# Optimization experiments

Hardware: AMD Instinct MI355X
Metric: run time of the kernel (lower is better)

Reference implementation:

```python
import jax, jax.numpy as jnp
import numpy as np

S, N, C, E, L = 4, 50000, 256, 800000, 3
EPS = 1e-5  # nn.LayerNorm default eps


def setup_inputs() -> dict:
    key = jax.random.key(0)
    ks = jax.random.split(key, 10)
    sc = 1.0 / np.sqrt(C)
    x = jax.random.normal(ks[0], (S, N, C), jnp.float32)
    edge_index = jax.random.randint(ks[1], (S, 2, E), 0, N, dtype=jnp.int32)
    edge_weight = jax.random.uniform(ks[2], (S, E), jnp.float32)
    W_gcn = jax.random.uniform(ks[3], (L, C, C), jnp.float32, -sc, sc)
    b_gcn = jnp.zeros((L, C), jnp.float32)
    ln_scale = jnp.ones((L, C), jnp.float32)
    ln_bias = jnp.zeros((L, C), jnp.float32)
    w_ih = jax.random.uniform(ks[4], (3 * C, C), jnp.float32, -sc, sc)
    w_hh = jax.random.uniform(ks[5], (3 * C, C), jnp.float32, -sc, sc)
    b_ih = jax.random.uniform(ks[6], (3 * C,), jnp.float32, -sc, sc)
    b_hh = jax.random.uniform(ks[7], (3 * C,), jnp.float32, -sc, sc)
    return dict(x=x, edge_index=edge_index, edge_weight=edge_weight,
                W_gcn=W_gcn, b_gcn=b_gcn, ln_scale=ln_scale, ln_bias=ln_bias,
                w_ih=w_ih, w_hh=w_hh, b_ih=b_ih, b_hh=b_hh)


def _gcn_conv(h, row, col, ew, W, b):
    """PyG GCNConv: out = D^{-1/2} (A + I) D^{-1/2} (h W) + b, edge weights ew."""
    h = h @ W  # [N, C]
    loop = jnp.arange(N, dtype=row.dtype)
    row = jnp.concatenate([row, loop])
    col = jnp.concatenate([col, loop])
    ew = jnp.concatenate([ew, jnp.ones((N,), ew.dtype)])
    deg = jax.ops.segment_sum(ew, col, num_segments=N)  # in-degree at targets
    dinv = jnp.where(deg > 0, jax.lax.rsqrt(jnp.maximum(deg, EPS * 0 + 1e-12)), 0.0)
    norm = dinv[row] * ew * dinv[col]  # [E+N]
    msg = h[row] * norm[:, None]       # gather from sources
    return jax.ops.segment_sum(msg, col, num_segments=N) + b


def _layernorm(h, scale, bias):
    mu = jnp.mean(h, axis=-1, keepdims=True)
    var = jnp.mean(jnp.square(h - mu), axis=-1, keepdims=True)
    return (h - mu) * jax.lax.rsqrt(var + EPS) * scale + bias


def _snapshot(x, ei, ew, W_gcn, b_gcn, ln_scale, ln_bias):
    h = x
    row, col = ei[0], ei[1]
    for l in range(L):
        h = _gcn_conv(h, row, col, ew, W_gcn[l], b_gcn[l])
        h = _layernorm(h, ln_scale[l], ln_bias[l])
        h = jax.nn.relu(h)  # dropout is identity in eval mode
    return h


def _gru_last(seq, w_ih, w_hh, b_ih, b_hh):
    """seq: [S, N, C] -> final hidden [N, C] (torch single-layer GRU)."""
    def step(h, x_t):
        gi = x_t @ w_ih.T + b_ih
        gh = h @ w_hh.T + b_hh
        i_r, i_z, i_n = jnp.split(gi, 3, axis=-1)
        h_r, h_z, h_n = jnp.split(gh, 3, axis=-1)
        r = jax.nn.sigmoid(i_r + h_r)
        z = jax.nn.sigmoid(i_z + h_z)
        n = jnp.tanh(i_n + r * h_n)
        return (1.0 - z) * n + z * h, None
    h0 = jnp.zeros(seq.shape[1:], seq.dtype)
    h_last, _ = jax.lax.scan(step, h0, seq)
    return h_last


def reference(x, edge_index, edge_weight, W_gcn, b_gcn, ln_scale, ln_bias,
              w_ih, w_hh, b_ih, b_hh):
    feats = jax.vmap(lambda xs, eis, ews: _snapshot(xs, eis, ews, W_gcn, b_gcn, ln_scale, ln_bias))(
        x, edge_index, edge_weight)  # [S, N, C]
    return _gru_last(feats, w_ih, w_hh, b_ih, b_hh)  # [N, C]
```

## Files before the change

kernel.cpp:

```cpp
#include <hip/hip_runtime.h>
#include <cmath>

#define S_ 4
#define N_ 50000
#define C_ 256
#define E_ 800000
#define L_ 3
#define EPS_ 1e-5f
#define NCH_ ((N_ + 1023) / 1024)

typedef __attribute__((ext_vector_type(8))) short bf16x8;
typedef __attribute__((ext_vector_type(4))) float f32x4;

__device__ __forceinline__ float bf2f(unsigned short s) {
  return __uint_as_float(((unsigned)s) << 16);
}
__device__ __forceinline__ unsigned short f2bf(float f) {
  unsigned u = __float_as_uint(f);
  return (unsigned short)((u + 0x7fffu + ((u >> 16) & 1u)) >> 16);
}

__device__ __forceinline__ void gload_lds16(const void* g, void* l) {
  __builtin_amdgcn_global_load_lds(
      (const __attribute__((address_space(1))) unsigned int*)g,
      (__attribute__((address_space(3))) unsigned int*)l, 16, 0, 0);
}

__device__ __forceinline__ void swz_block(int id, int nbx, int nby, int& bmi, int& bni) {
  const int NB8 = nby * 8;
  int fullb = (nbx >> 3) * NB8;
  if (id < fullb) {
    int g = id / NB8, pp = id - g * NB8;
    bmi = g * 8 + (pp & 7);
    bni = pp >> 3;
  } else {
    int rem = nbx & 7;
    int idp = id - fullb;
    bmi = (nbx & ~7) + idp % rem;
    bni = idp / rem;
  }
}

__global__ __launch_bounds__(256) void gemm_bf16_kernel(
    const unsigned short* __restrict__ A, const unsigned short* __restrict__ Bt,
    unsigned short* __restrict__ Cout, int M, int Nn, int K, int nby)
{
  __shared__ alignas(16) unsigned short As[2][128 * 32];
  __shared__ alignas(16) unsigned short Bs[2][128 * 32];
  const int tid = threadIdx.x;
  const int lane = tid & 63;
  const int wid = tid >> 6;
  const int wr = wid >> 1, wc = wid & 1;
  int bmi, bni;
  swz_block(blockIdx.x, gridDim.x / nby, nby, bmi, bni);
  const int bm = bmi * 128, bn = bni * 128;
  const int l15 = lane & 15, l4 = lane >> 4;

  f32x4 acc[4][4] = {};

  int offA[4], offB[4];
  #pragma unroll
  for (int mi = 0; mi < 4; ++mi) {
    int ra = wr * 64 + mi * 16 + l15;
    offA[mi] = ra * 32 + ((l4 ^ ((ra >> 1) & 3)) << 3);
    int rb = wc * 64 + mi * 16 + l15;
    offB[mi] = rb * 32 + ((l4 ^ ((rb >> 1) & 3)) << 3);
  }
  const int rs = tid >> 2;
  const int gs = tid & 3;

  auto stage = [&](int buf, int k0) {
    #pragma unroll
    for (int t2 = 0; t2 < 2; ++t2) {
      int r = rs + t2 * 64;
      int q = gs ^ ((r >> 1) & 3);
      int arow = bm + r; if (arow >= M) arow = M - 1;
      gload_lds16(&A[(size_t)arow * K + k0 + q * 8], &As[buf][(t2 * 256 + tid) * 8]);
      int brow = bn + r;
      gload_lds16(&Bt[(size_t)brow * K + k0 + q * 8], &Bs[buf][(t2 * 256 + tid) * 8]);
    }
  };

  const int nt = K >> 5;
  stage(0, 0);
  asm volatile("s_waitcnt vmcnt(0)" ::: "memory");
  __syncthreads();

  int cur = 0;
  for (int t = 0; t < nt; ++t) {
    if (t + 1 < nt) stage(cur ^ 1, (t + 1) * 32);

    bf16x8 af[4], bfr[4];
    #pragma unroll
    for (int mi = 0; mi < 4; ++mi) af[mi] = *(const bf16x8*)&As[cur][offA[mi]];
    #pragma unroll
    for (int ni = 0; ni < 4; ++ni) bfr[ni] = *(const bf16x8*)&Bs[cur][offB[ni]];
    #pragma unroll
    for (int mi = 0; mi < 4; ++mi)
      #pragma unroll
      for (int ni = 0; ni < 4; ++ni)
        acc[mi][ni] = __builtin_amdgcn_mfma_f32_16x16x32_bf16(
            af[mi], bfr[ni], acc[mi][ni], 0, 0, 0);

    asm volatile("s_waitcnt vmcnt(0)" ::: "memory");
    __syncthreads();
    cur ^= 1;
  }

  #pragma unroll
  for (int mi = 0; mi < 4; ++mi) {
    int rowb = bm + wr * 64 + mi * 16 + l4 * 4;
    #pragma unroll
    for (int ni = 0; ni < 4; ++ni) {
      int col = bn + wc * 64 + ni * 16 + l15;
      #pragma unroll
      for (int r = 0; r < 4; ++r) {
        int row = rowb + r;
        if (row < M) Cout[(size_t)row * Nn + col] = f2bf(acc[mi][ni][r]);
      }
    }
  }
}

__global__ __launch_bounds__(256) void gru_fused_kernel(
    const unsigned short* __restrict__ feat,
    const unsigned short* __restrict__ hq_in,
    const unsigned short* __restrict__ Wp_ih,
    const unsigned short* __restrict__ Wp_hh,
    const float* __restrict__ b_ih, const float* __restrict__ b_hh,
    unsigned short* __restrict__ hq_out, float* __restrict__ hout,
    int first, int M)
{
  __shared__ alignas(16) unsigned short As[2][128 * 32];
  __shared__ alignas(16) unsigned short Bs[2][96 * 32];
  const int tid = threadIdx.x;
  const int lane = tid & 63;
  const int wv = tid >> 6;
  const int l15 = lane & 15, l4 = lane >> 4;

  int bmi, bni;
  swz_block(blockIdx.x, gridDim.x / 8, 8, bmi, bni);
  const int bm = bmi * 128;
  const int c0 = bni * 32;
  const int brow0 = bni * 96;

  f32x4 acc_i[2][6] = {};
  f32x4 acc_h[2][6] = {};

  int offA[2], offB[6];
  #pragma unroll
  for (int mi = 0; mi < 2; ++mi) {
    int ra = wv * 32 + mi * 16 + l15;
    offA[mi] = ra * 32 + ((l4 ^ ((ra >> 1) & 3)) << 3);
  }
  #pragma unroll
  for (int ni = 0; ni < 6; ++ni) {
    int rb = ni * 16 + l15;
    offB[ni] = rb * 32 + ((l4 ^ ((rb >> 1) & 3)) << 3);
  }

  const int nt = first ? 8 : 16;

  auto stage = [&](int buf, int t) {
    int k0 = (t & 7) * 32;
    const unsigned short* Ap = (t < 8) ? feat : hq_in;
    const unsigned short* Bp = (t < 8) ? Wp_ih : Wp_hh;
    #pragma unroll
    for (int t2 = 0; t2 < 2; ++t2) {
      int slot = t2 * 256 + tid;
      int r = slot >> 2;
      int q = (slot & 3) ^ ((r >> 1) & 3);
      int arow = bm + r; if (arow >= M) arow = M - 1;
      gload_lds16(&Ap[(size_t)arow * 256 + k0 + q * 8], &As[buf][slot * 8]);
    }
    {
      int slot = tid;
      int r = slot >> 2;
      int q = (slot & 3) ^ ((r >> 1) & 3);
      gload_lds16(&Bp[(size_t)(brow0 + r) * 256 + k0 + q * 8], &Bs[buf][slot * 8]);
    }
    if (tid < 128) {
      int slot = 256 + tid;
      int r = slot >> 2;
      int q = (slot & 3) ^ ((r >> 1) & 3);
      gload_lds16(&Bp[(size_t)(brow0 + r) * 256 + k0 + q * 8], &Bs[buf][slot * 8]);
    }
  };

  stage(0, 0);
  asm volatile("s_waitcnt vmcnt(0)" ::: "memory");
  __syncthreads();

  int cur = 0;
  for (int t = 0; t < nt; ++t) {
    if (t + 1 < nt) stage(cur ^ 1, t + 1);

    bf16x8 af[2], bfr[6];
    #pragma unroll
    for (int mi = 0; mi < 2; ++mi) af[mi] = *(const bf16x8*)&As[cur][offA[mi]];
    #pragma unroll
    for (int ni = 0; ni < 6; ++ni) bfr[ni] = *(const bf16x8*)&Bs[cur][offB[ni]];
    if (t < 8) {
      #pragma unroll
      for (int mi = 0; mi < 2; ++mi)
        #pragma unroll
        for (int ni = 0; ni < 6; ++ni)
          acc_i[mi][ni] = __builtin_amdgcn_mfma_f32_16x16x32_bf16(
              af[mi], bfr[ni], acc_i[mi][ni], 0, 0, 0);
    } else {
      #pragma unroll
      for (int mi = 0; mi < 2; ++mi)
        #pragma unroll
        for (int ni = 0; ni < 6; ++ni)
          acc_h[mi][ni] = __builtin_amdgcn_mfma_f32_16x16x32_bf16(
              af[mi], bfr[ni], acc_h[mi][ni], 0, 0, 0);
    }

    asm volatile("s_waitcnt vmcnt(0)" ::: "memory");
    __syncthreads();
    cur ^= 1;
  }

  #pragma unroll
  for (int cni = 0; cni < 2; ++cni) {
    int c = c0 + cni * 16 + l15;
    float bir = b_ih[c], biz = b_ih[256 + c], bin = b_ih[512 + c];
    float bhr = b_hh[c], bhz = b_hh[256 + c], bhn = b_hh[512 + c];
    #pragma unroll
    for (int mi = 0; mi < 2; ++mi) {
      int rowb = bm + wv * 32 + mi * 16 + l4 * 4;
      #pragma unroll
      for (int rr = 0; rr < 4; ++rr) {
        int row = rowb + rr;
        if (row < M) {
          float gir = acc_i[mi][0 + cni][rr] + bir;
          float ghr = acc_h[mi][0 + cni][rr] + bhr;
          float giz = acc_i[mi][2 + cni][rr] + biz;
          float ghz = acc_h[mi][2 + cni][rr] + bhz;
          float gin = acc_i[mi][4 + cni][rr] + bin;
          float ghn = acc_h[mi][4 + cni][rr] + bhn;
          float rg = 1.f / (1.f + expf(-(gir + ghr)));
          float zg = 1.f / (1.f + expf(-(giz + ghz)));
          float ng = tanhf(gin + rg * ghn);
          float hp = first ? 0.f : bf2f(hq_in[(size_t)row * 256 + c]);
          float hv = (1.f - zg) * ng + zg * hp;
          if (hq_out) hq_out[(size_t)row * 256 + c] = f2bf(hv);
          if (hout) hout[(size_t)row * 256 + c] = hv;
        }
      }
    }
  }
}

__global__ void prep_wgcn_kernel(const float* __restrict__ W, unsigned short* __restrict__ Wt) {
  int i = blockIdx.x * blockDim.x + threadIdx.x;
  if (i < L_ * C_ * C_) {
    int l = i / (C_ * C_);
    int rem = i - l * C_ * C_;
    int nn = rem >> 8, k = rem & 255;
    Wt[i] = f2bf(W[l * C_ * C_ + k * C_ + nn]);
  }
}
__global__ void prep_wp_kernel(const float* __restrict__ W, unsigned short* __restrict__ Wp) {
  int d = blockIdx.x * blockDim.x + threadIdx.x;
  if (d < 768 * 256) {
    int jrow = d >> 8, k = d & 255;
    int chunk = jrow / 96, j = jrow - chunk * 96;
    int g = j >> 5, dc = j & 31;
    int srow = g * 256 + chunk * 32 + dc;
    Wp[d] = f2bf(W[srow * 256 + k]);
  }
}
__global__ void quant_kernel(const float* __restrict__ in, unsigned short* __restrict__ out, int n4) {
  int i = blockIdx.x * blockDim.x + threadIdx.x;
  if (i < n4) {
    float4 v = ((const float4*)in)[i];
    ushort4 q;
    q.x = f2bf(v.x); q.y = f2bf(v.y); q.z = f2bf(v.z); q.w = f2bf(v.w);
    *(ushort4*)&out[i * 4] = q;
  }
}

__global__ void init_kernel(unsigned long long* __restrict__ deg64,
                            int* __restrict__ fill, int n) {
  int i = blockIdx.x * blockDim.x + threadIdx.x;
  if (i < n) { deg64[i] = (1ULL << 20); fill[i] = 0; }
}
__global__ void deg_count_all_kernel(const int* __restrict__ edge_idx,
                                     const float* __restrict__ edge_w,
                                     unsigned long long* __restrict__ deg64) {
  int e = blockIdx.x * blockDim.x + threadIdx.x;
  if (e < S_ * E_) {
    int s = e / E_;
    int ee = e - s * E_;
    int c = edge_idx[(size_t)s * 2 * E_ + E_ + ee];
    float w = edge_w[(size_t)s * E_ + ee];
    unsigned long long q = (unsigned long long)__float2uint_rn(w * 1048576.0f);
    atomicAdd(&deg64[s * N_ + c], q + (1ULL << 40));
  }
}
__global__ void dinv_kernel(const unsigned long long* __restrict__ deg64,
                            float* __restrict__ dinv, int n) {
  int i = blockIdx.x * blockDim.x + threadIdx.x;
  if (i < n) {
    float d = (float)(deg64[i] & ((1ULL << 40) - 1)) * (1.0f / 1048576.0f);
    dinv[i] = rsqrtf(fmaxf(d, 1e-12f));
  }
}
__global__ void chunk_sum_kernel(const unsigned long long* __restrict__ deg64,
                                 int* __restrict__ chunk_sum) {
  int b = blockIdx.x;
  int s = b / NCH_, ch = b - s * NCH_;
  const unsigned long long* dg = deg64 + (size_t)s * N_;
  int base = ch * 1024 + threadIdx.x * 4;
  int v = 0;
  #pragma unroll
  for (int j = 0; j < 4; ++j)
    if (base + j < N_) v += (int)(dg[base + j] >> 40);
  #pragma unroll
  for (int off = 32; off > 0; off >>= 1) v += __shfl_down(v, off);
  __shared__ int ws[4];
  int lane = threadIdx.x & 63, wv = threadIdx.x >> 6;
  if (lane == 0) ws[wv] = v;
  __syncthreads();
  if (threadIdx.x == 0) chunk_sum[s * NCH_ + ch] = ws[0] + ws[1] + ws[2] + ws[3];
}
__global__ void scan_chunks_kernel(int* __restrict__ chunk_sum, int* __restrict__ rowptr) {
  int s = threadIdx.x;
  if (s < S_) {
    int tot = 0;
    for (int ch = 0; ch < NCH_; ++ch) {
      int t = chunk_sum[s * NCH_ + ch];
      chunk_sum[s * NCH_ + ch] = tot;
      tot += t;
    }
    rowptr[s * (N_ + 1) + N_] = tot;
  }
}
__global__ void scan_final_kernel(const unsigned long long* __restrict__ deg64,
                                  const int* __restrict__ chunk_sum,
                                  int* __restrict__ rowptr) {
  int b = blockIdx.x;
  int s = b / NCH_, ch = b - s * NCH_;
  const unsigned long long* dg = deg64 + (size_t)s * N_;
  int t = threadIdx.x;
  int i0 = ch * 1024 + t * 4;
  int c0 = 0, c1 = 0, c2 = 0, c3 = 0;
  if (i0 + 0 < N_) c0 = (int)(dg[i0 + 0] >> 40);
  if (i0 + 1 < N_) c1 = (int)(dg[i0 + 1] >> 40);
  if (i0 + 2 < N_) c2 = (int)(dg[i0 + 2] >> 40);
  if (i0 + 3 < N_) c3 = (int)(dg[i0 + 3] >> 40);
  int tsum = c0 + c1 + c2 + c3;
  int lane = t & 63, wv = t >> 6;
  int inc = tsum;
  #pragma unroll
  for (int off = 1; off < 64; off <<= 1) {
    int u = __shfl_up(inc, off);
    if (lane >= off) inc += u;
  }
  __shared__ int ws[4];
  if (lane == 63) ws[wv] = inc;
  __syncthreads();
  int woff = 0;
  for (int k = 0; k < 4; ++k) if (k < wv) woff += ws[k];
  int off0 = chunk_sum[s * NCH_ + ch] + woff + inc - tsum;
  int* rp = rowptr + (size_t)s * (N_ + 1);
  if (i0 + 0 < N_) rp[i0 + 0] = off0;
  if (i0 + 1 < N_) rp[i0 + 1] = off0 + c0;
  if (i0 + 2 < N_) rp[i0 + 2] = off0 + c0 + c1;
  if (i0 + 3 < N_) rp[i0 + 3] = off0 + c0 + c1 + c2;
}
__global__ void csr_fill_all_kernel(const int* __restrict__ edge_idx,
                                    const float* __restrict__ edge_w,
                                    const float* __restrict__ dinv,
                                    const int* __restrict__ rowptr, int* __restrict__ fill,
                                    unsigned int* __restrict__ src_norm) {
  int e = blockIdx.x * blockDim.x + threadIdx.x;
  if (e < S_ * E_) {
    int s = e / E_;
    int ee = e - s * E_;
    int r = edge_idx[(size_t)s * 2 * E_ + ee];
    int c = edge_idx[(size_t)s * 2 * E_ + E_ + ee];
    float w = edge_w[(size_t)s * E_ + ee];
    int pos = rowptr[s * (N_ + 1) + c] + atomicAdd(&fill[s * N_ + c], 1);
    float nrm = dinv[s * N_ + r] * w * dinv[s * N_ + c];
    unsigned int rec = (unsigned int)r | ((unsigned int)f2bf(nrm) << 16);
    src_norm[(size_t)s * E_ + pos] = rec;
  }
}

__global__ __launch_bounds__(256) void spmm_ln_relu_kernel(
    const unsigned short* __restrict__ hW, const int* __restrict__ rowptr,
    const unsigned int* __restrict__ src_norm,
    const float* __restrict__ dinv, const float* __restrict__ bgcn,
    const float* __restrict__ lnsc, const float* __restrict__ lnbi,
    unsigned short* __restrict__ out)
{
  const int tid = threadIdx.x;
  const int lane = tid & 63, wv = tid >> 6;
  const int n = blockIdx.x * 4 + wv;
  const int c4 = lane << 2;

  float a0, a1, a2, a3;
  {
    float dv = dinv[n];
    float w = dv * dv;
    ushort4 u = *(const ushort4*)&hW[((size_t)n << 8) + c4];
    a0 = w * bf2f(u.x); a1 = w * bf2f(u.y); a2 = w * bf2f(u.z); a3 = w * bf2f(u.w);
  }
  const int e0 = rowptr[n], e1 = rowptr[n + 1];
  for (int base = e0; base < e1; base += 64) {
    int cnt = min(64, e1 - base);
    unsigned int rec = (base + lane < e1) ? src_norm[base + lane] : 0u;
    int j = 0;
    for (; j + 3 < cnt; j += 4) {
      unsigned int r0 = __shfl((int)rec, j + 0);
      unsigned int r1 = __shfl((int)rec, j + 1);
      unsigned int r2 = __shfl((int)rec, j + 2);
      unsigned int r3 = __shfl((int)rec, j + 3);
      ushort4 u0 = *(const ushort4*)&hW[((size_t)(r0 & 0xFFFFu) << 8) + c4];
      ushort4 u1 = *(const ushort4*)&hW[((size_t)(r1 & 0xFFFFu) << 8) + c4];
      ushort4 u2 = *(const ushort4*)&hW[((size_t)(r2 & 0xFFFFu) << 8) + c4];
      ushort4 u3 = *(const ushort4*)&hW[((size_t)(r3 & 0xFFFFu) << 8) + c4];
      float n0 = bf2f((unsigned short)(r0 >> 16));
      float n1 = bf2f((unsigned short)(r1 >> 16));
      float n2 = bf2f((unsigned short)(r2 >> 16));
      float n3 = bf2f((unsigned short)(r3 >> 16));
      a0 = fmaf(n0, bf2f(u0.x), a0); a1 = fmaf(n0, bf2f(u0.y), a1);
      a2 = fmaf(n0, bf2f(u0.z), a2); a3 = fmaf(n0, bf2f(u0.w), a3);
      a0 = fmaf(n1, bf2f(u1.x), a0); a1 = fmaf(n1, bf2f(u1.y), a1);
      a2 = fmaf(n1, bf2f(u1.z), a2); a3 = fmaf(n1, bf2f(u1.w), a3);
      a0 = fmaf(n2, bf2f(u2.x), a0); a1 = fmaf(n2, bf2f(u2.y), a1);
      a2 = fmaf(n2, bf2f(u2.z), a2); a3 = fmaf(n2, bf2f(u2.w), a3);
      a0 = fmaf(n3, bf2f(u3.x), a0); a1 = fmaf(n3, bf2f(u3.y), a1);
      a2 = fmaf(n3, bf2f(u3.z), a2); a3 = fmaf(n3, bf2f(u3.w), a3);
    }
    for (; j < cnt; ++j) {
      unsigned int r0 = __shfl((int)rec, j);
      ushort4 u0 = *(const ushort4*)&hW[((size_t)(r0 & 0xFFFFu) << 8) + c4];
      float n0 = bf2f((unsigned short)(r0 >> 16));
      a0 = fmaf(n0, bf2f(u0.x), a0); a1 = fmaf(n0, bf2f(u0.y), a1);
      a2 = fmaf(n0, bf2f(u0.z), a2); a3 = fmaf(n0, bf2f(u0.w), a3);
    }
  }

  float4 bg = *(const float4*)&bgcn[c4];
  float v0 = a0 + bg.x, v1 = a1 + bg.y, v2 = a2 + bg.z, v3 = a3 + bg.w;
  float s1 = (v0 + v1) + (v2 + v3);
  float s2 = (v0 * v0 + v1 * v1) + (v2 * v2 + v3 * v3);
  #pragma unroll
  for (int off = 32; off > 0; off >>= 1) {
    s1 += __shfl_xor(s1, off);
    s2 += __shfl_xor(s2, off);
  }
  float mu = s1 * (1.0f / C_);
  float var = s2 * (1.0f / C_) - mu * mu;
  float inv = rsqrtf(var + EPS_);
  float4 sc = *(const float4*)&lnsc[c4];
  float4 bi = *(const float4*)&lnbi[c4];
  ushort4 o;
  o.x = f2bf(fmaxf((v0 - mu) * inv * sc.x + bi.x, 0.f));
  o.y = f2bf(fmaxf((v1 - mu) * inv * sc.y + bi.y, 0.f));
  o.z = f2bf(fmaxf((v2 - mu) * inv * sc.z + bi.z, 0.f));
  o.w = f2bf(fmaxf((v3 - mu) * inv * sc.w + bi.w, 0.f));
  *(ushort4*)&out[((size_t)n << 8) + c4] = o;
}

extern "C" void kernel_launch(void* const* d_in, const int* in_sizes, int n_in,
                              void* d_out, int out_size, void* d_ws, size_t ws_size,
                              hipStream_t stream) {
  const float* x        = (const float*)d_in[0];
  const int*   edge_idx = (const int*)d_in[1];
  const float* edge_w   = (const float*)d_in[2];
  const float* W_gcn    = (const float*)d_in[3];
  const float* b_gcn    = (const float*)d_in[4];
  const float* ln_scale = (const float*)d_in[5];
  const float* ln_bias  = (const float*)d_in[6];
  const float* w_ih     = (const float*)d_in[7];
  const float* w_hh     = (const float*)d_in[8];
  const float* b_ih     = (const float*)d_in[9];
  const float* b_hh     = (const float*)d_in[10];
  float* h_out = (float*)d_out;

  char* p = (char*)d_ws;
  auto carve = [&](size_t bytes) -> void* {
    void* r = (void*)p;
    p += (bytes + 255) & ~(size_t)255;
    return r;
  };
  unsigned long long* deg64 = (unsigned long long*)carve((size_t)S_ * N_ * 8);
  float* dinv        = (float*)carve((size_t)S_ * N_ * 4);
  int*   fill        = (int*)carve((size_t)S_ * N_ * 4);
  int*   rowptr      = (int*)carve((size_t)S_ * (N_ + 1) * 4);
  int*   chunk_sum   = (int*)carve((size_t)S_ * NCH_ * 4);
  unsigned int* src_norm = (unsigned int*)carve((size_t)S_ * E_ * 4);
  unsigned short* wt_gcn = (unsigned short*)carve((size_t)L_ * C_ * C_ * 2);
  unsigned short* wp_ih  = (unsigned short*)carve((size_t)768 * C_ * 2);
  unsigned short* wp_hh  = (unsigned short*)carve((size_t)768 * C_ * 2);
  unsigned short* xq_all = (unsigned short*)carve((size_t)S_ * N_ * C_ * 2);
  unsigned short* hW_all = (unsigned short*)carve((size_t)S_ * N_ * C_ * 2);
  unsigned short* fA_all = (unsigned short*)carve((size_t)S_ * N_ * C_ * 2);
  unsigned short* hq0    = (unsigned short*)carve((size_t)N_ * C_ * 2);
  unsigned short* hq1    = (unsigned short*)carve((size_t)N_ * C_ * 2);

  const int TB = 256;

  prep_wgcn_kernel<<<(L_ * C_ * C_ + TB - 1) / TB, TB, 0, stream>>>(W_gcn, wt_gcn);
  prep_wp_kernel<<<(768 * C_ + TB - 1) / TB, TB, 0, stream>>>(w_ih, wp_ih);
  prep_wp_kernel<<<(768 * C_ + TB - 1) / TB, TB, 0, stream>>>(w_hh, wp_hh);

  quant_kernel<<<((size_t)S_ * N_ * C_ / 4 + TB - 1) / TB, TB, 0, stream>>>(
      x, xq_all, S_ * N_ * C_ / 4);

  init_kernel<<<(S_ * N_ + TB - 1) / TB, TB, 0, stream>>>(deg64, fill, S_ * N_);
  deg_count_all_kernel<<<(S_ * E_ + TB - 1) / TB, TB, 0, stream>>>(edge_idx, edge_w, deg64);
  dinv_kernel<<<(S_ * N_ + TB - 1) / TB, TB, 0, stream>>>(deg64, dinv, S_ * N_);
  chunk_sum_kernel<<<S_ * NCH_, TB, 0, stream>>>(deg64, chunk_sum);
  scan_chunks_kernel<<<1, 64, 0, stream>>>(chunk_sum, rowptr);
  scan_final_kernel<<<S_ * NCH_, TB, 0, stream>>>(deg64, chunk_sum, rowptr);
  csr_fill_all_kernel<<<(S_ * E_ + TB - 1) / TB, TB, 0, stream>>>(
      edge_idx, edge_w, dinv, rowptr, fill, src_norm);

  const int M_all = S_ * N_;
  const int nbx = (M_all + 127) / 128;
  {
    const unsigned short* hin = xq_all;
    for (int l = 0; l < L_; ++l) {
      unsigned short* fout = (l == 1) ? xq_all : fA_all;
      gemm_bf16_kernel<<<nbx * (C_ / 128), 256, 0, stream>>>(
          hin, wt_gcn + (size_t)l * C_ * C_, hW_all, M_all, C_, C_, C_ / 128);
      for (int s = 0; s < S_; ++s) {
        spmm_ln_relu_kernel<<<N_ / 4, 256, 0, stream>>>(
            hW_all + (size_t)s * N_ * C_, rowptr + s * (N_ + 1),
            src_norm + (size_t)s * E_,
            dinv + s * N_, b_gcn + l * C_,
            ln_scale + l * C_, ln_bias + l * C_, fout + (size_t)s * N_ * C_);
      }
      hin = fout;
    }
  }
  const unsigned short* feat_all = fA_all;

  const int gnb = ((N_ + 127) / 128) * 8;
  unsigned short* hq_cur = hq0;
  unsigned short* hq_nxt = hq1;
  for (int s = 0; s < S_; ++s) {
    bool last = (s == S_ - 1);
    gru_fused_kernel<<<gnb, 256, 0, stream>>>(
        feat_all + (size_t)s * N_ * C_,
        hq_cur,
        wp_ih, wp_hh, b_ih, b_hh,
        last ? nullptr : hq_nxt,
        last ? h_out : nullptr,
        (s == 0) ? 1 : 0, N_);
    unsigned short* t = hq_cur; hq_cur = hq_nxt; hq_nxt = t;
  }
}
```

Baseline: 1.678 ms.

## Build CSR via column-bucketed binning with shared-memory atomics; batch SpMM across snapshots

Replaces the global-atomic degree count and CSR fill with a two-pass bucket sort. Edges are first binned by column block into per-bucket sub-bins. Per-bucket kernels then count degrees and fill CSR positions using LDS atomics, and compute dinv locally. The four per-snapshot SpMM launches are also merged into one launch over all snapshots. This costs a large fixed-capacity bin buffer and silently drops edges if a sub-bin overflows CAP8.

```diff
diff --git a/kernel.cpp b/kernel.cpp
--- a/kernel.cpp
+++ b/kernel.cpp
@@ -8,6 +8,11 @@
 #define L_ 3
 #define EPS_ 1e-5f
 #define NCH_ ((N_ + 1023) / 1024)
+#define BKT_SH 9
+#define BKT_SZ 512
+#define NBKT ((N_ + BKT_SZ - 1) / BKT_SZ)
+#define NSUB 8
+#define CAP8 2048
 
 typedef __attribute__((ext_vector_type(8))) short bf16x8;
 typedef __attribute__((ext_vector_type(4))) float f32x4;
@@ -281,42 +286,70 @@
   }
 }
 
-__global__ void init_kernel(unsigned long long* __restrict__ deg64,
-                            int* __restrict__ fill, int n) {
-  int i = blockIdx.x * blockDim.x + threadIdx.x;
-  if (i < n) { deg64[i] = (1ULL << 20); fill[i] = 0; }
-}
-__global__ void deg_count_all_kernel(const int* __restrict__ edge_idx,
-                                     const float* __restrict__ edge_w,
-                                     unsigned long long* __restrict__ deg64) {
+__global__ void bin_kernel(const int* __restrict__ edge_idx,
+                           const float* __restrict__ edge_w,
+                           unsigned long long* __restrict__ bins,
+                           int* __restrict__ bfill) {
   int e = blockIdx.x * blockDim.x + threadIdx.x;
   if (e < S_ * E_) {
     int s = e / E_;
     int ee = e - s * E_;
+    int r = edge_idx[(size_t)s * 2 * E_ + ee];
     int c = edge_idx[(size_t)s * 2 * E_ + E_ + ee];
     float w = edge_w[(size_t)s * E_ + ee];
-    unsigned long long q = (unsigned long long)__float2uint_rn(w * 1048576.0f);
-    atomicAdd(&deg64[s * N_ + c], q + (1ULL << 40));
-  }
-}
-__global__ void dinv_kernel(const unsigned long long* __restrict__ deg64,
-                            float* __restrict__ dinv, int n) {
-  int i = blockIdx.x * blockDim.x + threadIdx.x;
-  if (i < n) {
-    float d = (float)(deg64[i] & ((1ULL << 40) - 1)) * (1.0f / 1048576.0f);
-    dinv[i] = rsqrtf(fmaxf(d, 1e-12f));
-  }
-}
-__global__ void chunk_sum_kernel(const unsigned long long* __restrict__ deg64,
+    int sb = (s * NBKT + (c >> BKT_SH)) * NSUB + (blockIdx.x & (NSUB - 1));
+    int pos = atomicAdd(&bfill[sb], 1);
+    if (pos < CAP8) {
+      unsigned long long rec = ((unsigned long long)__float_as_uint(w) << 32)
+          | (unsigned int)(r | ((c & (BKT_SZ - 1)) << 16));
+      bins[(size_t)sb * CAP8 + pos] = rec;
+    }
+  }
+}
+
+__global__ __launch_bounds__(256) void bucket_stats_kernel(
+    const unsigned long long* __restrict__ bins, const int* __restrict__ bfill,
+    int* __restrict__ cnt_g, float* __restrict__ dinv_g) {
+  __shared__ unsigned int lcnt[BKT_SZ], lwd[BKT_SZ];
+  int b = blockIdx.x;
+  int s = b / NBKT, bl = b - s * NBKT;
+  int col0 = bl << BKT_SH;
+  for (int i = threadIdx.x; i < BKT_SZ; i += 256) { lcnt[i] = 0; lwd[i] = 0; }
+  __syncthreads();
+  for (int sub = 0; sub < NSUB; ++sub) {
+    int sb = b * NSUB + sub;
+    int nb = min(bfill[sb], CAP8);
+    const unsigned long long* bp = bins + (size_t)sb * CAP8;
+    for (int e = threadIdx.x; e < nb; e += 256) {
+      unsigned long long rec = bp[e];
+      unsigned int lo = (unsigned int)rec;
+      int cl = (lo >> 16) & (BKT_SZ - 1);
+      float w = __uint_as_float((unsigned int)(rec >> 32));
+      atomicAdd(&lcnt[cl], 1u);
+      atomicAdd(&lwd[cl], (unsigned int)__float2uint_rn(w * 1048576.0f));
+    }
+  }
+  __syncthreads();
+  for (int i = threadIdx.x; i < BKT_SZ; i += 256) {
+    int c = col0 + i;
+    if (c < N_) {
+      cnt_g[s * N_ + c] = (int)lcnt[i];
+      float d = (float)lwd[i] * (1.0f / 1048576.0f) + 1.0f;
+      dinv_g[s * N_ + c] = rsqrtf(d);
+    }
+  }
+}
+
+__global__ void chunk_sum_kernel(const int* __restrict__ cnt_g,
                                  int* __restrict__ chunk_sum) {
   int b = blockIdx.x;
   int s = b / NCH_, ch = b - s * NCH_;
-  const unsigned long long* dg = deg64 + (size_t)s * N_;
+  const int* cs = cnt_g + (size_t)s * N_;
   int base = ch * 1024 + threadIdx.x * 4;
   int v = 0;
   #pragma unroll
   for (int j = 0; j < 4; ++j)
-    if (base + j < N_) v += (int)(dg[base + j] >> 40);
+    if (base + j < N_) v += cs[base + j];
   #pragma unroll
   for (int off = 32; off > 0; off >>= 1) v += __shfl_down(v, off);
   __shared__ int ws[4];
@@ -337,19 +370,19 @@
     rowptr[s * (N_ + 1) + N_] = tot;
   }
 }
-__global__ void scan_final_kernel(const unsigned long long* __restrict__ deg64,
+__global__ void scan_final_kernel(const int* __restrict__ cnt_g,
                                   const int* __restrict__ chunk_sum,
                                   int* __restrict__ rowptr) {
   int b = blockIdx.x;
   int s = b / NCH_, ch = b - s * NCH_;
-  const unsigned long long* dg = deg64 + (size_t)s * N_;
+  const int* cs = cnt_g + (size_t)s * N_;
   int t = threadIdx.x;
   int i0 = ch * 1024 + t * 4;
   int c0 = 0, c1 = 0, c2 = 0, c3 = 0;
-  if (i0 + 0 < N_) c0 = (int)(dg[i0 + 0] >> 40);
-  if (i0 + 1 < N_) c1 = (int)(dg[i0 + 1] >> 40);
-  if (i0 + 2 < N_) c2 = (int)(dg[i0 + 2] >> 40);
-  if (i0 + 3 < N_) c3 = (int)(dg[i0 + 3] >> 40);
+  if (i0 + 0 < N_) c0 = cs[i0 + 0];
+  if (i0 + 1 < N_) c1 = cs[i0 + 1];
+  if (i0 + 2 < N_) c2 = cs[i0 + 2];
+  if (i0 + 3 < N_) c3 = cs[i0 + 3];
   int tsum = c0 + c1 + c2 + c3;
   int lane = t & 63, wv = t >> 6;
   int inc = tsum;
@@ -370,48 +403,69 @@
   if (i0 + 2 < N_) rp[i0 + 2] = off0 + c0 + c1;
   if (i0 + 3 < N_) rp[i0 + 3] = off0 + c0 + c1 + c2;
 }
-__global__ void csr_fill_all_kernel(const int* __restrict__ edge_idx,
-                                    const float* __restrict__ edge_w,
-                                    const float* __restrict__ dinv,
-                                    const int* __restrict__ rowptr, int* __restrict__ fill,
-                                    unsigned int* __restrict__ src_norm) {
-  int e = blockIdx.x * blockDim.x + threadIdx.x;
-  if (e < S_ * E_) {
-    int s = e / E_;
-    int ee = e - s * E_;
-    int r = edge_idx[(size_t)s * 2 * E_ + ee];
-    int c = edge_idx[(size_t)s * 2 * E_ + E_ + ee];
-    float w = edge_w[(size_t)s * E_ + ee];
-    int pos = rowptr[s * (N_ + 1) + c] + atomicAdd(&fill[s * N_ + c], 1);
-    float nrm = dinv[s * N_ + r] * w * dinv[s * N_ + c];
-    unsigned int rec = (unsigned int)r | ((unsigned int)f2bf(nrm) << 16);
-    src_norm[(size_t)s * E_ + pos] = rec;
+
+__global__ __launch_bounds__(256) void csr_build_kernel(
+    const unsigned long long* __restrict__ bins, const int* __restrict__ bfill,
+    const float* __restrict__ dinv_g, const int* __restrict__ rowptr,
+    unsigned int* __restrict__ src_norm) {
+  __shared__ int lfill[BKT_SZ];
+  __shared__ float ldinv[BKT_SZ];
+  int b = blockIdx.x;
+  int s = b / NBKT, bl = b - s * NBKT;
+  int col0 = bl << BKT_SH;
+  for (int i = threadIdx.x; i < BKT_SZ; i += 256) {
+    lfill[i] = 0;
+    int c = col0 + i;
+    ldinv[i] = (c < N_) ? dinv_g[s * N_ + c] : 0.f;
+  }
+  __syncthreads();
+  const float* dvs = dinv_g + (size_t)s * N_;
+  const int* rp = rowptr + (size_t)s * (N_ + 1);
+  unsigned int* sn = src_norm + (size_t)s * E_;
+  for (int sub = 0; sub < NSUB; ++sub) {
+    int sb = b * NSUB + sub;
+    int nb = min(bfill[sb], CAP8);
+    const unsigned long long* bp = bins + (size_t)sb * CAP8;
+    for (int e = threadIdx.x; e < nb; e += 256) {
+      unsigned long long rec = bp[e];
+      unsigned int lo = (unsigned int)rec;
+      int src = lo & 0xFFFF;
+      int cl = (lo >> 16) & (BKT_SZ - 1);
+      float w = __uint_as_float((unsigned int)(rec >> 32));
+      float nrm = dvs[src] * w * ldinv[cl];
+      int pos = rp[col0 + cl] + atomicAdd(&lfill[cl], 1);
+      sn[pos] = (unsigned int)src | ((unsigned int)f2bf(nrm) << 16);
+    }
   }
 }
 
 __global__ __launch_bounds__(256) void spmm_ln_relu_kernel(
-    const unsigned short* __restrict__ hW, const int* __restrict__ rowptr,
-    const unsigned int* __restrict__ src_norm,
-    const float* __restrict__ dinv, const float* __restrict__ bgcn,
-    const float* __restrict__ lnsc, const float* __restrict__ lnbi,
-    unsigned short* __restrict__ out)
+    const unsigned short* __restrict__ hW_all, const int* __restrict__ rowptr,
+    const unsigned int* __restrict__ src_norm, const float* __restrict__ dinv_g,
+    const float* __restrict__ bgcn, const float* __restrict__ lnsc,
+    const float* __restrict__ lnbi, unsigned short* __restrict__ out)
 {
   const int tid = threadIdx.x;
   const int lane = tid & 63, wv = tid >> 6;
-  const int n = blockIdx.x * 4 + wv;
+  const int n_g = blockIdx.x * 4 + wv;
+  const int s = n_g / N_;
+  const int n = n_g - s * N_;
   const int c4 = lane << 2;
+  const unsigned short* hW = hW_all + ((size_t)s * N_ << 8);
+  const unsigned int* sn = src_norm + (size_t)s * E_;
+  const int* rp = rowptr + (size_t)s * (N_ + 1);
 
   float a0, a1, a2, a3;
   {
-    float dv = dinv[n];
+    float dv = dinv_g[n_g];
     float w = dv * dv;
     ushort4 u = *(const ushort4*)&hW[((size_t)n << 8) + c4];
     a0 = w * bf2f(u.x); a1 = w * bf2f(u.y); a2 = w * bf2f(u.z); a3 = w * bf2f(u.w);
   }
-  const int e0 = rowptr[n], e1 = rowptr[n + 1];
+  const int e0 = rp[n], e1 = rp[n + 1];
   for (int base = e0; base < e1; base += 64) {
     int cnt = min(64, e1 - base);
-    unsigned int rec = (base + lane < e1) ? src_norm[base + lane] : 0u;
+    unsigned int rec = (base + lane < e1) ? sn[base + lane] : 0u;
     int j = 0;
     for (; j + 3 < cnt; j += 4) {
       unsigned int r0 = __shfl((int)rec, j + 0);
@@ -463,7 +517,7 @@
   o.y = f2bf(fmaxf((v1 - mu) * inv * sc.y + bi.y, 0.f));
   o.z = f2bf(fmaxf((v2 - mu) * inv * sc.z + bi.z, 0.f));
   o.w = f2bf(fmaxf((v3 - mu) * inv * sc.w + bi.w, 0.f));
-  *(ushort4*)&out[((size_t)n << 8) + c4] = o;
+  *(ushort4*)&out[((size_t)n_g << 8) + c4] = o;
 }
 
 extern "C" void kernel_launch(void* const* d_in, const int* in_sizes, int n_in,
@@ -488,9 +542,10 @@
     p += (bytes + 255) & ~(size_t)255;
     return r;
   };
-  unsigned long long* deg64 = (unsigned long long*)carve((size_t)S_ * N_ * 8);
-  float* dinv        = (float*)carve((size_t)S_ * N_ * 4);
-  int*   fill        = (int*)carve((size_t)S_ * N_ * 4);
+  unsigned long long* bins = (unsigned long long*)carve((size_t)S_ * NBKT * NSUB * CAP8 * 8);
+  int*   bfill       = (int*)carve((size_t)S_ * NBKT * NSUB * 4);
+  int*   cnt_g       = (int*)carve((size_t)S_ * N_ * 4);
+  float* dinv_g      = (float*)carve((size_t)S_ * N_ * 4);
   int*   rowptr      = (int*)carve((size_t)S_ * (N_ + 1) * 4);
   int*   chunk_sum   = (int*)carve((size_t)S_ * NCH_ * 4);
   unsigned int* src_norm = (unsigned int*)carve((size_t)S_ * E_ * 4);
@@ -505,6 +560,8 @@
 
   const int TB = 256;
 
+  hipMemsetAsync(bfill, 0, (size_t)S_ * NBKT * NSUB * 4, stream);
+
   prep_wgcn_kernel<<<(L_ * C_ * C_ + TB - 1) / TB, TB, 0, stream>>>(W_gcn, wt_gcn);
   prep_wp_kernel<<<(768 * C_ + TB - 1) / TB, TB, 0, stream>>>(w_ih, wp_ih);
   prep_wp_kernel<<<(768 * C_ + TB - 1) / TB, TB, 0, stream>>>(w_hh, wp_hh);
@@ -512,14 +569,12 @@
   quant_kernel<<<((size_t)S_ * N_ * C_ / 4 + TB - 1) / TB, TB, 0, stream>>>(
       x, xq_all, S_ * N_ * C_ / 4);
 
-  init_kernel<<<(S_ * N_ + TB - 1) / TB, TB, 0, stream>>>(deg64, fill, S_ * N_);
-  deg_count_all_kernel<<<(S_ * E_ + TB - 1) / TB, TB, 0, stream>>>(edge_idx, edge_w, deg64);
-  dinv_kernel<<<(S_ * N_ + TB - 1) / TB, TB, 0, stream>>>(deg64, dinv, S_ * N_);
-  chunk_sum_kernel<<<S_ * NCH_, TB, 0, stream>>>(deg64, chunk_sum);
+  bin_kernel<<<(S_ * E_ + TB - 1) / TB, TB, 0, stream>>>(edge_idx, edge_w, bins, bfill);
+  bucket_stats_kernel<<<S_ * NBKT, TB, 0, stream>>>(bins, bfill, cnt_g, dinv_g);
+  chunk_sum_kernel<<<S_ * NCH_, TB, 0, stream>>>(cnt_g, chunk_sum);
   scan_chunks_kernel<<<1, 64, 0, stream>>>(chunk_sum, rowptr);
-  scan_final_kernel<<<S_ * NCH_, TB, 0, stream>>>(deg64, chunk_sum, rowptr);
-  csr_fill_all_kernel<<<(S_ * E_ + TB - 1) / TB, TB, 0, stream>>>(
-      edge_idx, edge_w, dinv, rowptr, fill, src_norm);
+  scan_final_kernel<<<S_ * NCH_, TB, 0, stream>>>(cnt_g, chunk_sum, rowptr);
+  csr_build_kernel<<<S_ * NBKT, TB, 0, stream>>>(bins, bfill, dinv_g, rowptr, src_norm);
 
   const int M_all = S_ * N_;
   const int nbx = (M_all + 127) / 128;
@@ -529,13 +584,9 @@
       unsigned short* fout = (l == 1) ? xq_all : fA_all;
       gemm_bf16_kernel<<<nbx * (C_ / 128), 256, 0, stream>>>(
           hin, wt_gcn + (size_t)l * C_ * C_, hW_all, M_all, C_, C_, C_ / 128);
-      for (int s = 0; s < S_; ++s) {
-        spmm_ln_relu_kernel<<<N_ / 4, 256, 0, stream>>>(
-            hW_all + (size_t)s * N_ * C_, rowptr + s * (N_ + 1),
-            src_norm + (size_t)s * E_,
-            dinv + s * N_, b_gcn + l * C_,
-            ln_scale + l * C_, ln_bias + l * C_, fout + (size_t)s * N_ * C_);
-      }
+      spmm_ln_relu_kernel<<<M_all / 4, 256, 0, stream>>>(
+          hW_all, rowptr, src_norm, dinv_g, b_gcn + l * C_,
+          ln_scale + l * C_, ln_bias + l * C_, fout);
       hin = fout;
     }
   }
```

Measured after the change: 2.193 ms. 30.7% more time.
